# Performance work log

Measured on AMD Instinct MI355X. Metric: run time of the kernel, lower is better.

Reference implementation:

```python
import jax, jax.numpy as jnp
import numpy as np

B, C_IN, C_OUT, H, W = 4, 256, 256, 64, 64
KH = KW = 3
STRIDE = 1
PAD = 1
DIL = 1


def setup_inputs() -> dict:
    key = jax.random.key(0)
    k1, k2, k3, k4 = jax.random.split(key, 4)
    x = jax.random.normal(k1, (B, C_IN, H, W), dtype=jnp.float32)
    # torchvision layout: 2*dg*KH*KW channels, (y, x) pair per kernel tap
    offset = jax.random.normal(k2, (B, 2 * KH * KW, H, W), dtype=jnp.float32)
    fan_in = C_IN * KH * KW
    weight = jax.random.normal(k3, (C_OUT, C_IN, KH, KW), dtype=jnp.float32) / np.sqrt(fan_in)
    bias = jax.random.normal(k4, (C_OUT,), dtype=jnp.float32) * 0.01
    return {"x": x, "offset": offset, "weight": weight, "bias": bias}


def _gather_bilinear_corner(x_flat, yi, xi, h, w):
    # x_flat: [B, C, H*W]; yi/xi: [B, KK, Ho, Wo] int32
    valid = ((yi >= 0) & (yi < h) & (xi >= 0) & (xi < w)).astype(x_flat.dtype)
    idx = jnp.clip(yi, 0, h - 1) * w + jnp.clip(xi, 0, w - 1)
    b = idx.shape[0]
    g = jnp.take_along_axis(x_flat, idx.reshape(b, 1, -1), axis=2)
    return g.reshape(b, x_flat.shape[1], *yi.shape[1:]), valid


def deform_conv2d(x, offset, weight, bias):
    b, c, h, w = x.shape
    o = weight.shape[0]
    kk = KH * KW
    ho = (h + 2 * PAD - DIL * (KH - 1) - 1) // STRIDE + 1
    wo = (w + 2 * PAD - DIL * (KW - 1) - 1) // STRIDE + 1

    ky = (jnp.arange(kk, dtype=jnp.float32) // KW) * DIL  # [KK]
    kx = (jnp.arange(kk, dtype=jnp.float32) % KW) * DIL
    hs = jnp.arange(ho, dtype=jnp.float32) * STRIDE - PAD   # [Ho]
    ws = jnp.arange(wo, dtype=jnp.float32) * STRIDE - PAD   # [Wo]

    off = offset.reshape(b, kk, 2, ho, wo)
    py = hs[None, None, :, None] + ky[None, :, None, None] + off[:, :, 0]  # [B,KK,Ho,Wo]
    px = ws[None, None, None, :] + kx[None, :, None, None] + off[:, :, 1]

    y0 = jnp.floor(py)
    x0 = jnp.floor(px)
    wy1 = py - y0  # fractional parts, differentiable w.r.t. offsets
    wx1 = px - x0
    wy0 = 1.0 - wy1
    wx0 = 1.0 - wx1
    y0i = y0.astype(jnp.int32)
    x0i = x0.astype(jnp.int32)

    x_flat = x.reshape(b, c, h * w)
    corners = [
        (y0i,     x0i,     wy0 * wx0),
        (y0i,     x0i + 1, wy0 * wx1),
        (y0i + 1, x0i,     wy1 * wx0),
        (y0i + 1, x0i + 1, wy1 * wx1),
    ]
    sampled = jnp.zeros((b, c, kk, ho, wo), dtype=x.dtype)
    for yi, xi, wgt in corners:
        g, valid = _gather_bilinear_corner(x_flat, yi, xi, h, w)
        sampled = sampled + g * (wgt * valid)[:, None]

    out = jnp.einsum('bckhw,ock->bohw', sampled, weight.reshape(o, c, kk))
    return out + bias[None, :, None, None]


def reference(x, offset, weight, bias):
    return deform_conv2d(x, offset, weight, bias)
```

## Files before the change

### kernel.cpp

```cpp
#include <hip/hip_runtime.h>

typedef __bf16 bf16;
typedef __bf16 bf16x4 __attribute__((ext_vector_type(4)));
typedef __bf16 bf16x8 __attribute__((ext_vector_type(8)));
typedef float  f32x4  __attribute__((ext_vector_type(4)));
typedef float  f32x16 __attribute__((ext_vector_type(16)));
typedef unsigned int u32x4 __attribute__((ext_vector_type(4)));

#define KK     9
#define KDIM   2304
#define KSTEPS 144
#define PXW    32

__device__ __forceinline__ int sreadi(int v) {
    return __builtin_amdgcn_readfirstlane(v);
}

__device__ __forceinline__ float BL(unsigned v) {
    return __builtin_bit_cast(float, v << 16);
}
__device__ __forceinline__ float BH(unsigned v) {
    return __builtin_bit_cast(float, v & 0xffff0000u);
}

__global__ __launch_bounds__(256) void prep2_k(const float* __restrict__ x,
                                               const float* __restrict__ w,
                                               bf16* __restrict__ xt,
                                               bf16* __restrict__ wq) {
    __shared__ __align__(16) char smem[8 * 2308 * 2];
    int bid = blockIdx.x;
    int tid = threadIdx.x;
    if (bid < 1024) {
        float (*tileF)[65] = reinterpret_cast<float(*)[65]>(smem);
        int pt = bid & 63, ct = (bid >> 6) & 3, b = bid >> 8;
        const float* src = x + ((size_t)(b * 256 + ct * 64)) * 4096 + pt * 64;
        int f4 = tid & 15;
        int cl = tid >> 4;
        #pragma unroll
        for (int q = 0; q < 4; ++q) {
            int c = q * 16 + cl;
            f32x4 v = *reinterpret_cast<const f32x4*>(src + (size_t)c * 4096 + f4 * 4);
            tileF[f4 * 4 + 0][c] = v[0];
            tileF[f4 * 4 + 1][c] = v[1];
            tileF[f4 * 4 + 2][c] = v[2];
            tileF[f4 * 4 + 3][c] = v[3];
        }
        __syncthreads();
        int j = tid & 7, p0 = tid >> 3;
        bf16* dst = xt + ((size_t)(b * 4096 + pt * 64)) * 256 + ct * 64 + j * 8;
        #pragma unroll
        for (int pp = 0; pp < 2; ++pp) {
            int p = p0 + pp * 32;
            bf16x8 sv;
            #pragma unroll
            for (int k = 0; k < 8; ++k) sv[k] = (bf16)tileF[p][j * 8 + k];
            *reinterpret_cast<bf16x8*>(dst + (size_t)p * 256) = sv;
        }
    } else {
        bf16 (*Wl)[2308] = reinterpret_cast<bf16(*)[2308]>(smem);
        int wb     = bid - 1024;
        int o_base = wb * 8;
        int m      = o_base >> 5;
        int o31b   = o_base & 31;
        #pragma unroll
        for (int pass = 0; pass < 18; ++pass) {
            int i    = pass * 256 + tid;
            int r    = i / 576;
            int col4 = i - r * 576;
            f32x4 v = *reinterpret_cast<const f32x4*>(
                w + (size_t)(o_base + r) * KDIM + col4 * 4);
            Wl[r][col4 * 4 + 0] = (bf16)v[0];
            Wl[r][col4 * 4 + 1] = (bf16)v[1];
            Wl[r][col4 * 4 + 2] = (bf16)v[2];
            Wl[r][col4 * 4 + 3] = (bf16)v[3];
        }
        __syncthreads();
        #pragma unroll
        for (int pass = 0; pass < 9; ++pass) {
            int gid  = pass * 256 + tid;
            int ol   = gid & 7;
            int half = (gid >> 3) & 1;
            int ks   = gid >> 4;
            int kb   = ks * 16 + half * 8;
            int tap  = kb >> 8;
            int cc0  = kb & 255;
            bf16x8 sv;
            #pragma unroll
            for (int j = 0; j < 8; ++j) sv[j] = Wl[ol][(cc0 + j) * 9 + tap];
            size_t g = (size_t)((m * KSTEPS + ks) * 64 + half * 32 + o31b + ol);
            *reinterpret_cast<bf16x8*>(wq + g * 8) = sv;
        }
    }
}

__global__ __launch_bounds__(1024, 8) void deform_gemm_k(
    const bf16*  __restrict__ xt,
    const float* __restrict__ off,
    const bf16*  __restrict__ wq,
    const float* __restrict__ bias,
    float*       __restrict__ out) {

    __shared__ bf16 S[2][PXW * 256];

    int tid   = threadIdx.x;
    int wavei = sreadi(tid >> 6);
    int lane  = tid & 63;
    int l32   = lane & 31;
    int half  = lane >> 5;
    int mt    = wavei & 7;
    int kh    = wavei >> 3;

    int bid   = blockIdx.x;
    int pb    = ((bid & 7) << 6) | (bid >> 3);
    int pix0  = pb * PXW;
    int b     = pix0 >> 12;
    int pimgb = pix0 & 4095;
    int obase = b * 73728;
    int rot   = ((bid >> 3) & 1) * 4;

    int n     = wavei * 2 + half;
    int pimg  = pimgb + n;
    int py_i  = pimg >> 6, px_i = pimg & 63;
    const char* xb = (const char*)xt + ((size_t)b << 21) + l32 * 16;

    f32x16 acc;
    #pragma unroll
    for (int r = 0; r < 16; ++r) acc[r] = 0.f;

    float oyC = off[obase + (2 * rot) * 4096 + pimg];
    float oxC = off[obase + (2 * rot + 1) * 4096 + pimg];

    for (int t = 0; t < KK; ++t) {
        int tap = t + rot; if (tap >= KK) tap -= KK;
        int ty = tap / 3 - 1;
        int tx = tap % 3 - 1;
        bf16* Sw = &S[t & 1][0];

        float py = (float)(py_i + ty) + oyC;
        float px = (float)(px_i + tx) + oxC;
        float fy = floorf(py), fx = floorf(px);
        int   y0 = (int)fy,    x0 = (int)fx;
        float wy1 = py - fy, wx1 = px - fx;
        float wy0 = 1.f - wy1, wx0 = 1.f - wx1;
        wy0 = ((unsigned)y0       < 64u) ? wy0 : 0.f;
        wy1 = ((unsigned)(y0 + 1) < 64u) ? wy1 : 0.f;
        wx0 = ((unsigned)x0       < 64u) ? wx0 : 0.f;
        wx1 = ((unsigned)(x0 + 1) < 64u) ? wx1 : 0.f;
        int yc0 = min(max(y0, 0), 63), yc1 = min(max(y0 + 1, 0), 63);
        int xc0 = min(max(x0, 0), 63), xc1 = min(max(x0 + 1, 0), 63);
        unsigned u0 = (unsigned)(yc0 * 64 + xc0) * 512u;
        unsigned u1 = (unsigned)(yc0 * 64 + xc1) * 512u;
        unsigned u2 = (unsigned)(yc1 * 64 + xc0) * 512u;
        unsigned u3 = (unsigned)(yc1 * 64 + xc1) * 512u;
        float w0 = wy0 * wx0, w1 = wy0 * wx1;
        float w2 = wy1 * wx0, w3 = wy1 * wx1;
        u32x4 g0 = *(const u32x4*)(xb + u0);
        u32x4 g1 = *(const u32x4*)(xb + u1);
        u32x4 g2 = *(const u32x4*)(xb + u2);
        u32x4 g3 = *(const u32x4*)(xb + u3);
        bf16x8 sv;
        #pragma unroll
        for (int q = 0; q < 4; ++q) {
            float lo = fmaf(w0, BL(g0[q]), fmaf(w1, BL(g1[q]),
                       fmaf(w2, BL(g2[q]),      w3 * BL(g3[q]))));
            float hi = fmaf(w0, BH(g0[q]), fmaf(w1, BH(g1[q]),
                       fmaf(w2, BH(g2[q]),      w3 * BH(g3[q]))));
            sv[q * 2]     = (bf16)lo;
            sv[q * 2 + 1] = (bf16)hi;
        }
        int gsw = l32 ^ (n & 31);
        *reinterpret_cast<bf16x8*>(Sw + n * 256 + gsw * 8) = sv;

        const bf16* ap0 = wq +
            ((size_t)(((mt * KSTEPS) + tap * 16 + kh * 8) * 64 + lane)) * 8;
        bf16x8 a0 = *reinterpret_cast<const bf16x8*>(ap0);
        bf16x8 a1 = *reinterpret_cast<const bf16x8*>(ap0 + 512);
        bf16x8 a2 = *reinterpret_cast<const bf16x8*>(ap0 + 1024);
        bf16x8 a3 = *reinterpret_cast<const bf16x8*>(ap0 + 1536);

        __syncthreads();

        if (t < KK - 1) {
            int tn = tap + 1; if (tn >= KK) tn = 0;
            oyC = off[obase + (2 * tn) * 4096 + pimg];
            oxC = off[obase + (2 * tn + 1) * 4096 + pimg];
        }

        const bf16* Sr = Sw;
        #pragma unroll
        for (int kk2 = 0; kk2 < 8; ++kk2) {
            bf16x8 a;
            if      (kk2 == 0) a = a0;
            else if (kk2 == 1) a = a1;
            else if (kk2 == 2) a = a2;
            else if (kk2 == 3) a = a3;
            else a = *reinterpret_cast<const bf16x8*>(ap0 + (size_t)kk2 * 512);
            int s  = kh * 8 + kk2;
            int g  = s * 2 + half;
            int gs = g ^ l32;
            bf16x8 bv = *reinterpret_cast<const bf16x8*>(Sr + l32 * 256 + gs * 8);
            acc = __builtin_amdgcn_mfma_f32_32x32x16_bf16(a, bv, acc, 0, 0, 0);
        }
    }

    __syncthreads();
    float* Sf = reinterpret_cast<float*>(&S[0][0]);
    if (wavei >= 8) {
        int wb = (wavei - 8) * 64 + lane;
        #pragma unroll
        for (int r = 0; r < 16; ++r)
            Sf[r * 512 + wb] = acc[r];
    }
    __syncthreads();
    if (wavei < 8) {
        int wb   = wavei * 64 + lane;
        int m    = mt * 32;
        int pimo = pimgb + l32;
        float* op = out + ((size_t)(b * 256 + m)) * 4096 + pimo;
        #pragma unroll
        for (int r = 0; r < 16; ++r) {
            int row = (r & 3) + 8 * (r >> 2) + half * 4;
            float v = acc[r] + Sf[r * 512 + wb] + bias[m + row];
            op[(size_t)row * 4096] = v;
        }
    }
}

extern "C" void kernel_launch(void* const* d_in, const int* in_sizes, int n_in,
                              void* d_out, int out_size, void* d_ws, size_t ws_size,
                              hipStream_t stream) {
    const float* x    = (const float*)d_in[0];
    const float* off  = (const float*)d_in[1];
    const float* w    = (const float*)d_in[2];
    const float* bias = (const float*)d_in[3];
    float* out = (float*)d_out;

    bf16* wq = (bf16*)d_ws;
    bf16* xt = (bf16*)((char*)d_ws + (size_t)589824 * 2);

    prep2_k<<<1056, 256, 0, stream>>>(x, w, xt, wq);
    deform_gemm_k<<<512, 1024, 0, stream>>>(xt, off, wq, bias, out);
}
```

Before: 121.3 us.

## Double pixel tile per block so each weight fragment feeds two MFMAs

Widens each block's pixel tile from 32 to 64. Every wave now samples two pixels per tap and runs two 32x32 MFMA accumulators that share one weight fragment, which halves global weight loads per output and launches half as many blocks. All eight weight fragments are preloaded into registers, and the tap rotation now spans eight starting taps. The cost is more registers per thread (two accumulators plus eight A fragments), a lower occupancy hint, and only 256 blocks, which may underfill the GPU's compute units.

```diff
diff --git a/kernel.cpp b/kernel.cpp
--- a/kernel.cpp
+++ b/kernel.cpp
@@ -10,7 +10,7 @@
 #define KK     9
 #define KDIM   2304
 #define KSTEPS 144
-#define PXW    32
+#define PXW    64
 
 __device__ __forceinline__ int sreadi(int v) {
     return __builtin_amdgcn_readfirstlane(v);
@@ -93,7 +93,7 @@
     }
 }
 
-__global__ __launch_bounds__(1024, 8) void deform_gemm_k(
+__global__ __launch_bounds__(1024, 4) void deform_gemm_k(
     const bf16*  __restrict__ xt,
     const float* __restrict__ off,
     const bf16*  __restrict__ wq,
@@ -111,33 +111,27 @@
     int kh    = wavei >> 3;
 
     int bid   = blockIdx.x;
-    int pb    = ((bid & 7) << 6) | (bid >> 3);
+    int pb    = ((bid & 7) << 5) | (bid >> 3);
     int pix0  = pb * PXW;
     int b     = pix0 >> 12;
     int pimgb = pix0 & 4095;
     int obase = b * 73728;
-    int rot   = ((bid >> 3) & 1) * 4;
-
-    int n     = wavei * 2 + half;
-    int pimg  = pimgb + n;
-    int py_i  = pimg >> 6, px_i = pimg & 63;
+    int rot   = (bid >> 3) & 7;
+
+    int n0    = wavei * 4 + half * 2;
+    int n1    = n0 + 1;
+    int pimg0 = pimgb + n0;
+    int pimg1 = pimgb + n1;
     const char* xb = (const char*)xt + ((size_t)b << 21) + l32 * 16;
 
-    f32x16 acc;
+    f32x16 acc0, acc1;
     #pragma unroll
-    for (int r = 0; r < 16; ++r) acc[r] = 0.f;
-
-    float oyC = off[obase + (2 * rot) * 4096 + pimg];
-    float oxC = off[obase + (2 * rot + 1) * 4096 + pimg];
-
-    for (int t = 0; t < KK; ++t) {
-        int tap = t + rot; if (tap >= KK) tap -= KK;
-        int ty = tap / 3 - 1;
-        int tx = tap % 3 - 1;
-        bf16* Sw = &S[t & 1][0];
-
-        float py = (float)(py_i + ty) + oyC;
-        float px = (float)(px_i + tx) + oxC;
+    for (int r = 0; r < 16; ++r) { acc0[r] = 0.f; acc1[r] = 0.f; }
+
+    auto body = [&](int n, int pimg, float oy, float ox, int ty, int tx,
+                    bf16* Sw) {
+        float py = (float)((pimg >> 6) + ty) + oy;
+        float px = (float)((pimg & 63) + tx) + ox;
         float fy = floorf(py), fx = floorf(px);
         int   y0 = (int)fy,    x0 = (int)fx;
         float wy1 = py - fy, wx1 = px - fx;
@@ -170,58 +164,76 @@
         }
         int gsw = l32 ^ (n & 31);
         *reinterpret_cast<bf16x8*>(Sw + n * 256 + gsw * 8) = sv;
+    };
+
+    float oy0 = off[obase + (2 * rot)     * 4096 + pimg0];
+    float ox0 = off[obase + (2 * rot + 1) * 4096 + pimg0];
+    float oy1 = off[obase + (2 * rot)     * 4096 + pimg1];
+    float ox1 = off[obase + (2 * rot + 1) * 4096 + pimg1];
+
+    for (int t = 0; t < KK; ++t) {
+        int tap = t + rot; if (tap >= KK) tap -= KK;
+        int ty = tap / 3 - 1;
+        int tx = tap % 3 - 1;
+        bf16* Sw = &S[t & 1][0];
+
+        body(n0, pimg0, oy0, ox0, ty, tx, Sw);
 
         const bf16* ap0 = wq +
             ((size_t)(((mt * KSTEPS) + tap * 16 + kh * 8) * 64 + lane)) * 8;
-        bf16x8 a0 = *reinterpret_cast<const bf16x8*>(ap0);
-        bf16x8 a1 = *reinterpret_cast<const bf16x8*>(ap0 + 512);
-        bf16x8 a2 = *reinterpret_cast<const bf16x8*>(ap0 + 1024);
-        bf16x8 a3 = *reinterpret_cast<const bf16x8*>(ap0 + 1536);
+        bf16x8 af[8];
+        #pragma unroll
+        for (int s = 0; s < 8; ++s)
+            af[s] = *reinterpret_cast<const bf16x8*>(ap0 + (size_t)s * 512);
+
+        body(n1, pimg1, oy1, ox1, ty, tx, Sw);
 
         __syncthreads();
 
         if (t < KK - 1) {
             int tn = tap + 1; if (tn >= KK) tn = 0;
-            oyC = off[obase + (2 * tn) * 4096 + pimg];
-            oxC = off[obase + (2 * tn + 1) * 4096 + pimg];
+            oy0 = off[obase + (2 * tn)     * 4096 + pimg0];
+            ox0 = off[obase + (2 * tn + 1) * 4096 + pimg0];
+            oy1 = off[obase + (2 * tn)     * 4096 + pimg1];
+            ox1 = off[obase + (2 * tn + 1) * 4096 + pimg1];
         }
 
         const bf16* Sr = Sw;
         #pragma unroll
-        for (int kk2 = 0; kk2 < 8; ++kk2) {
-            bf16x8 a;
-            if      (kk2 == 0) a = a0;
-            else if (kk2 == 1) a = a1;
-            else if (kk2 == 2) a = a2;
-            else if (kk2 == 3) a = a3;
-            else a = *reinterpret_cast<const bf16x8*>(ap0 + (size_t)kk2 * 512);
-            int s  = kh * 8 + kk2;
-            int g  = s * 2 + half;
+        for (int s = 0; s < 8; ++s) {
+            int g  = (kh * 8 + s) * 2 + half;
             int gs = g ^ l32;
-            bf16x8 bv = *reinterpret_cast<const bf16x8*>(Sr + l32 * 256 + gs * 8);
-            acc = __builtin_amdgcn_mfma_f32_32x32x16_bf16(a, bv, acc, 0, 0, 0);
+            bf16x8 b0 = *reinterpret_cast<const bf16x8*>(Sr + l32 * 256 + gs * 8);
+            bf16x8 b1 = *reinterpret_cast<const bf16x8*>(Sr + (32 + l32) * 256 + gs * 8);
+            acc0 = __builtin_amdgcn_mfma_f32_32x32x16_bf16(af[s], b0, acc0, 0, 0, 0);
+            acc1 = __builtin_amdgcn_mfma_f32_32x32x16_bf16(af[s], b1, acc1, 0, 0, 0);
         }
     }
 
     __syncthreads();
     float* Sf = reinterpret_cast<float*>(&S[0][0]);
-    if (wavei >= 8) {
-        int wb = (wavei - 8) * 64 + lane;
-        #pragma unroll
-        for (int r = 0; r < 16; ++r)
-            Sf[r * 512 + wb] = acc[r];
+    if (kh == 1) {
+        #pragma unroll
+        for (int r = 0; r < 16; ++r) {
+            Sf[((mt * 2 + 0) * 16 + r) * 64 + lane] = acc0[r];
+            Sf[((mt * 2 + 1) * 16 + r) * 64 + lane] = acc1[r];
+        }
     }
     __syncthreads();
-    if (wavei < 8) {
-        int wb   = wavei * 64 + lane;
-        int m    = mt * 32;
-        int pimo = pimgb + l32;
-        float* op = out + ((size_t)(b * 256 + m)) * 4096 + pimo;
-        #pragma unroll
-        for (int r = 0; r < 16; ++r) {
-            int row = (r & 3) + 8 * (r >> 2) + half * 4;
-            float v = acc[r] + Sf[r * 512 + wb] + bias[m + row];
-            op[(size_t)row * 4096] = v;
+    if (kh == 0) {
+        int m = mt * 32;
+        #pragma unroll
+        for (int nt = 0; nt < 2; ++nt) {
+            int px = pimgb + nt * 32 + l32;
+            float* op = out + ((size_t)(b * 256 + m)) * 4096 + px;
+            #pragma unroll
+            for (int r = 0; r < 16; ++r) {
+                int row = (r & 3) + 8 * (r >> 2) + half * 4;
+                float a = (nt == 0) ? acc0[r] : acc1[r];
+                float v = a + Sf[((mt * 2 + nt) * 16 + r) * 64 + lane]
+                            + bias[m + row];
+                op[(size_t)row * 4096] = v;
+            }
         }
     }
 }
@@ -239,5 +251,5 @@
     bf16* xt = (bf16*)((char*)d_ws + (size_t)589824 * 2);
 
     prep2_k<<<1056, 256, 0, stream>>>(x, w, xt, wq);
-    deform_gemm_k<<<512, 1024, 0, stream>>>(xt, off, wq, bias, out);
-}
+    deform_gemm_k<<<256, 1024, 0, stream>>>(xt, off, wq, bias, out);
+}
```

After: 113.2 us, median of 2. 6.7% less time.

## Gather all taps into shared memory before GEMM, two pixel tiles per block

Applied to the files above, without the earlier changes.

Each block now handles two 32-pixel tiles in sequence. For each tile it first samples all 9 taps into a 9-slot shared buffer, synchronises once, then runs the MFMA loop over all taps. This replaces the per-tap double-buffered interleaving of gather and MFMA, and it halves the grid to 256 blocks. It cuts barriers per tile, but gather and MFMA no longer overlap within a block. The larger LDS footprint (about 144KB) allows fewer resident blocks, and the tap rotation that spread weight reads across blocks is dropped.

```diff
diff --git a/kernel.cpp b/kernel.cpp
--- a/kernel.cpp
+++ b/kernel.cpp
@@ -1,7 +1,6 @@
 #include <hip/hip_runtime.h>
 
 typedef __bf16 bf16;
-typedef __bf16 bf16x4 __attribute__((ext_vector_type(4)));
 typedef __bf16 bf16x8 __attribute__((ext_vector_type(8)));
 typedef float  f32x4  __attribute__((ext_vector_type(4)));
 typedef float  f32x16 __attribute__((ext_vector_type(16)));
@@ -10,7 +9,7 @@
 #define KK     9
 #define KDIM   2304
 #define KSTEPS 144
-#define PXW    32
+#define PXT    32
 
 __device__ __forceinline__ int sreadi(int v) {
     return __builtin_amdgcn_readfirstlane(v);
@@ -93,14 +92,14 @@
     }
 }
 
-__global__ __launch_bounds__(1024, 8) void deform_gemm_k(
+__global__ __launch_bounds__(1024, 4) void deform_gemm_k(
     const bf16*  __restrict__ xt,
     const float* __restrict__ off,
     const bf16*  __restrict__ wq,
     const float* __restrict__ bias,
     float*       __restrict__ out) {
 
-    __shared__ bf16 S[2][PXW * 256];
+    __shared__ bf16 S[KK][PXT * 256];
 
     int tid   = threadIdx.x;
     int wavei = sreadi(tid >> 6);
@@ -110,119 +109,104 @@
     int mt    = wavei & 7;
     int kh    = wavei >> 3;
 
-    int bid   = blockIdx.x;
-    int pb    = ((bid & 7) << 6) | (bid >> 3);
-    int pix0  = pb * PXW;
-    int b     = pix0 >> 12;
-    int pimgb = pix0 & 4095;
-    int obase = b * 73728;
-    int rot   = ((bid >> 3) & 1) * 4;
-
-    int n     = wavei * 2 + half;
-    int pimg  = pimgb + n;
-    int py_i  = pimg >> 6, px_i = pimg & 63;
-    const char* xb = (const char*)xt + ((size_t)b << 21) + l32 * 16;
-
-    f32x16 acc;
-    #pragma unroll
-    for (int r = 0; r < 16; ++r) acc[r] = 0.f;
-
-    float oyC = off[obase + (2 * rot) * 4096 + pimg];
-    float oxC = off[obase + (2 * rot + 1) * 4096 + pimg];
-
-    for (int t = 0; t < KK; ++t) {
-        int tap = t + rot; if (tap >= KK) tap -= KK;
-        int ty = tap / 3 - 1;
-        int tx = tap % 3 - 1;
-        bf16* Sw = &S[t & 1][0];
-
-        float py = (float)(py_i + ty) + oyC;
-        float px = (float)(px_i + tx) + oxC;
-        float fy = floorf(py), fx = floorf(px);
-        int   y0 = (int)fy,    x0 = (int)fx;
-        float wy1 = py - fy, wx1 = px - fx;
-        float wy0 = 1.f - wy1, wx0 = 1.f - wx1;
-        wy0 = ((unsigned)y0       < 64u) ? wy0 : 0.f;
-        wy1 = ((unsigned)(y0 + 1) < 64u) ? wy1 : 0.f;
-        wx0 = ((unsigned)x0       < 64u) ? wx0 : 0.f;
-        wx1 = ((unsigned)(x0 + 1) < 64u) ? wx1 : 0.f;
-        int yc0 = min(max(y0, 0), 63), yc1 = min(max(y0 + 1, 0), 63);
-        int xc0 = min(max(x0, 0), 63), xc1 = min(max(x0 + 1, 0), 63);
-        unsigned u0 = (unsigned)(yc0 * 64 + xc0) * 512u;
-        unsigned u1 = (unsigned)(yc0 * 64 + xc1) * 512u;
-        unsigned u2 = (unsigned)(yc1 * 64 + xc0) * 512u;
-        unsigned u3 = (unsigned)(yc1 * 64 + xc1) * 512u;
-        float w0 = wy0 * wx0, w1 = wy0 * wx1;
-        float w2 = wy1 * wx0, w3 = wy1 * wx1;
-        u32x4 g0 = *(const u32x4*)(xb + u0);
-        u32x4 g1 = *(const u32x4*)(xb + u1);
-        u32x4 g2 = *(const u32x4*)(xb + u2);
-        u32x4 g3 = *(const u32x4*)(xb + u3);
-        bf16x8 sv;
-        #pragma unroll
-        for (int q = 0; q < 4; ++q) {
-            float lo = fmaf(w0, BL(g0[q]), fmaf(w1, BL(g1[q]),
-                       fmaf(w2, BL(g2[q]),      w3 * BL(g3[q]))));
-            float hi = fmaf(w0, BH(g0[q]), fmaf(w1, BH(g1[q]),
-                       fmaf(w2, BH(g2[q]),      w3 * BH(g3[q]))));
-            sv[q * 2]     = (bf16)lo;
-            sv[q * 2 + 1] = (bf16)hi;
-        }
-        int gsw = l32 ^ (n & 31);
-        *reinterpret_cast<bf16x8*>(Sw + n * 256 + gsw * 8) = sv;
-
-        const bf16* ap0 = wq +
-            ((size_t)(((mt * KSTEPS) + tap * 16 + kh * 8) * 64 + lane)) * 8;
-        bf16x8 a0 = *reinterpret_cast<const bf16x8*>(ap0);
-        bf16x8 a1 = *reinterpret_cast<const bf16x8*>(ap0 + 512);
-        bf16x8 a2 = *reinterpret_cast<const bf16x8*>(ap0 + 1024);
-        bf16x8 a3 = *reinterpret_cast<const bf16x8*>(ap0 + 1536);
-
-        __syncthreads();
-
-        if (t < KK - 1) {
-            int tn = tap + 1; if (tn >= KK) tn = 0;
-            oyC = off[obase + (2 * tn) * 4096 + pimg];
-            oxC = off[obase + (2 * tn + 1) * 4096 + pimg];
-        }
-
-        const bf16* Sr = Sw;
-        #pragma unroll
-        for (int kk2 = 0; kk2 < 8; ++kk2) {
-            bf16x8 a;
-            if      (kk2 == 0) a = a0;
-            else if (kk2 == 1) a = a1;
-            else if (kk2 == 2) a = a2;
-            else if (kk2 == 3) a = a3;
-            else a = *reinterpret_cast<const bf16x8*>(ap0 + (size_t)kk2 * 512);
-            int s  = kh * 8 + kk2;
-            int g  = s * 2 + half;
-            int gs = g ^ l32;
-            bf16x8 bv = *reinterpret_cast<const bf16x8*>(Sr + l32 * 256 + gs * 8);
-            acc = __builtin_amdgcn_mfma_f32_32x32x16_bf16(a, bv, acc, 0, 0, 0);
-        }
-    }
-
-    __syncthreads();
-    float* Sf = reinterpret_cast<float*>(&S[0][0]);
-    if (wavei >= 8) {
-        int wb = (wavei - 8) * 64 + lane;
-        #pragma unroll
-        for (int r = 0; r < 16; ++r)
-            Sf[r * 512 + wb] = acc[r];
-    }
-    __syncthreads();
-    if (wavei < 8) {
-        int wb   = wavei * 64 + lane;
-        int m    = mt * 32;
-        int pimo = pimgb + l32;
-        float* op = out + ((size_t)(b * 256 + m)) * 4096 + pimo;
-        #pragma unroll
-        for (int r = 0; r < 16; ++r) {
-            int row = (r & 3) + 8 * (r >> 2) + half * 4;
-            float v = acc[r] + Sf[r * 512 + wb] + bias[m + row];
-            op[(size_t)row * 4096] = v;
-        }
+    int bid = blockIdx.x;
+
+    for (int tt = 0; tt < 2; ++tt) {
+        int pblk  = ((bid & 7) << 6) | ((bid >> 3) << 1) | tt;
+        int pix0  = pblk * PXT;
+        int b     = pix0 >> 12;
+        int pimgb = pix0 & 4095;
+        int obase = b * 73728;
+
+        int n    = wavei * 2 + half;
+        int pimg = pimgb + n;
+        int py_i = pimg >> 6, px_i = pimg & 63;
+        const char* xb = (const char*)xt + ((size_t)b << 21) + l32 * 16;
+
+        for (int tap = 0; tap < KK; ++tap) {
+            int ty = tap / 3 - 1;
+            int tx = tap % 3 - 1;
+            float oy = off[obase + (2 * tap) * 4096 + pimg];
+            float ox = off[obase + (2 * tap + 1) * 4096 + pimg];
+            float py = (float)(py_i + ty) + oy;
+            float px = (float)(px_i + tx) + ox;
+            float fy = floorf(py), fx = floorf(px);
+            int   y0 = (int)fy,    x0 = (int)fx;
+            float wy1 = py - fy, wx1 = px - fx;
+            float wy0 = 1.f - wy1, wx0 = 1.f - wx1;
+            wy0 = ((unsigned)y0       < 64u) ? wy0 : 0.f;
+            wy1 = ((unsigned)(y0 + 1) < 64u) ? wy1 : 0.f;
+            wx0 = ((unsigned)x0       < 64u) ? wx0 : 0.f;
+            wx1 = ((unsigned)(x0 + 1) < 64u) ? wx1 : 0.f;
+            int yc0 = min(max(y0, 0), 63), yc1 = min(max(y0 + 1, 0), 63);
+            int xc0 = min(max(x0, 0), 63), xc1 = min(max(x0 + 1, 0), 63);
+            unsigned u0 = (unsigned)(yc0 * 64 + xc0) * 512u;
+            unsigned u1 = (unsigned)(yc0 * 64 + xc1) * 512u;
+            unsigned u2 = (unsigned)(yc1 * 64 + xc0) * 512u;
+            unsigned u3 = (unsigned)(yc1 * 64 + xc1) * 512u;
+            float w0 = wy0 * wx0, w1 = wy0 * wx1;
+            float w2 = wy1 * wx0, w3 = wy1 * wx1;
+            u32x4 g0 = *(const u32x4*)(xb + u0);
+            u32x4 g1 = *(const u32x4*)(xb + u1);
+            u32x4 g2 = *(const u32x4*)(xb + u2);
+            u32x4 g3 = *(const u32x4*)(xb + u3);
+            bf16x8 sv;
+            #pragma unroll
+            for (int q = 0; q < 4; ++q) {
+                float lo = fmaf(w0, BL(g0[q]), fmaf(w1, BL(g1[q]),
+                           fmaf(w2, BL(g2[q]),      w3 * BL(g3[q]))));
+                float hi = fmaf(w0, BH(g0[q]), fmaf(w1, BH(g1[q]),
+                           fmaf(w2, BH(g2[q]),      w3 * BH(g3[q]))));
+                sv[q * 2]     = (bf16)lo;
+                sv[q * 2 + 1] = (bf16)hi;
+            }
+            int gsw = l32 ^ n;
+            *reinterpret_cast<bf16x8*>(&S[tap][0] + n * 256 + gsw * 8) = sv;
+        }
+
+        __syncthreads();
+
+        f32x16 acc;
+        #pragma unroll
+        for (int r = 0; r < 16; ++r) acc[r] = 0.f;
+
+        for (int tap = 0; tap < KK; ++tap) {
+            const bf16* ap0 = wq +
+                ((size_t)(((mt * KSTEPS) + tap * 16 + kh * 8) * 64 + lane)) * 8;
+            const bf16* Sr = &S[tap][0];
+            #pragma unroll
+            for (int s = 0; s < 8; ++s) {
+                bf16x8 a = *reinterpret_cast<const bf16x8*>(ap0 + (size_t)s * 512);
+                int g  = (kh * 8 + s) * 2 + half;
+                int gs = g ^ l32;
+                bf16x8 bv = *reinterpret_cast<const bf16x8*>(Sr + l32 * 256 + gs * 8);
+                acc = __builtin_amdgcn_mfma_f32_32x32x16_bf16(a, bv, acc, 0, 0, 0);
+            }
+        }
+
+        __syncthreads();
+
+        float* Sf = reinterpret_cast<float*>(&S[0][0]);
+        if (kh == 1) {
+            int wb = (wavei - 8) * 64 + lane;
+            #pragma unroll
+            for (int r = 0; r < 16; ++r)
+                Sf[r * 512 + wb] = acc[r];
+        }
+        __syncthreads();
+        if (kh == 0) {
+            int wb   = wavei * 64 + lane;
+            int m    = mt * 32;
+            int pimo = pimgb + l32;
+            float* op = out + ((size_t)(b * 256 + m)) * 4096 + pimo;
+            #pragma unroll
+            for (int r = 0; r < 16; ++r) {
+                int row = (r & 3) + 8 * (r >> 2) + half * 4;
+                float v = acc[r] + Sf[r * 512 + wb] + bias[m + row];
+                op[(size_t)row * 4096] = v;
+            }
+        }
+        __syncthreads();
     }
 }
 
@@ -239,5 +223,5 @@
     bf16* xt = (bf16*)((char*)d_ws + (size_t)589824 * 2);
 
     prep2_k<<<1056, 256, 0, stream>>>(x, w, xt, wq);
-    deform_gemm_k<<<512, 1024, 0, stream>>>(xt, off, wq, bias, out);
-}
+    deform_gemm_k<<<256, 1024, 0, stream>>>(xt, off, wq, bias, out);
+}
```

Result: slower. 269.5 us (+122.1%).
